# Kernel optimization log

Measured on AMD Instinct MI355X. Metric: run time of the kernel, lower is better.

## Reference

```python
import jax, jax.numpy as jnp
import numpy as np

L = 2        # num_hidden_layers
B = 2        # batch
S = 1024     # seq_len
D = 2048     # hidden_size
H = 32       # num_attention_heads
HD = D // H  # head_dim = 64
I = 8192     # intermediate_size
EPS = 1e-5
INIT = 0.02


def setup_inputs() -> dict:
    key = jax.random.key(0)
    ks = jax.random.split(key, 12)
    r = lambda k, shape: jax.random.normal(k, shape, dtype=jnp.float32) * INIT
    return {
        "hidden_states": jax.random.normal(ks[0], (B, S, D), dtype=jnp.float32),
        "attention_mask": jnp.ones((B, S), dtype=jnp.int32),
        "ln1_g": jnp.ones((L, D), jnp.float32),
        "ln1_b": jnp.zeros((L, D), jnp.float32),
        "qkv_w": r(ks[1], (L, D, 3 * D)),
        "o_w": r(ks[2], (L, D, D)),
        "ln2_g": jnp.ones((L, D), jnp.float32),
        "ln2_b": jnp.zeros((L, D), jnp.float32),
        "gu_w": r(ks[3], (L, D, 2 * I)),
        "gu_b": jnp.zeros((L, 2 * I), jnp.float32),
        "down_w": r(ks[4], (L, I, D)),
        "down_b": jnp.zeros((L, D), jnp.float32),
    }


def _layer_norm(x, g, b):
    mu = jnp.mean(x, axis=-1, keepdims=True)
    var = jnp.mean(jnp.square(x - mu), axis=-1, keepdims=True)
    return (x - mu) * jax.lax.rsqrt(var + EPS) * g + b


def _forward(hidden_states, attention_mask, ln1_g, ln1_b, qkv_w, o_w,
             ln2_g, ln2_b, gu_w, gu_b, down_w, down_b):
    # mask bias: (1 - mask) * -1e4, broadcast to [B, 1, 1, S]
    mask_bias = (1.0 - attention_mask.astype(jnp.float32))[:, None, None, :] * -10000.0
    scale = 1.0 / np.sqrt(HD)

    def layer(h, p):
        l1g, l1b, qw, ow, l2g, l2b, guw, gub, dw, db = p
        # --- attention block ---
        x = _layer_norm(h, l1g, l1b)
        qkv = jnp.einsum("bsd,de->bse", x, qw)                 # [B,S,3D]
        qkv = qkv.reshape(B, S, 3, H, HD).transpose(2, 0, 3, 1, 4)  # [3,B,H,S,HD]
        q, k, v = qkv[0], qkv[1], qkv[2]
        scores = jnp.einsum("bhqd,bhkd->bhqk", q, k) * scale + mask_bias
        attn = jax.nn.softmax(scores, axis=-1)
        ctx = jnp.einsum("bhqk,bhkd->bhqd", attn, v)           # [B,H,S,HD]
        ctx = ctx.transpose(0, 2, 1, 3).reshape(B, S, D)
        h = h + jnp.einsum("bsd,de->bse", ctx, ow)
        # --- MLP block (SwiGLU) ---
        y = _layer_norm(h, l2g, l2b)
        gu = jnp.einsum("bsd,de->bse", y, guw) + gub           # [B,S,2I]
        gate, up = gu[..., :I], gu[..., I:]
        mlp = jnp.einsum("bsi,id->bsd", jax.nn.swish(gate) * up, dw) + db
        return h + mlp, None

    params = (ln1_g, ln1_b, qkv_w, o_w, ln2_g, ln2_b, gu_w, gu_b, down_w, down_b)
    out, _ = jax.lax.scan(layer, hidden_states, params)
    return out


def reference(hidden_states, attention_mask, ln1_g, ln1_b, qkv_w, o_w,
              ln2_g, ln2_b, gu_w, gu_b, down_w, down_b):
    return _forward(hidden_states, attention_mask, ln1_g, ln1_b, qkv_w, o_w,
                    ln2_g, ln2_b, gu_w, gu_b, down_w, down_b)
```

## Files before the change

### kernel.cpp

```cpp
#include <hip/hip_runtime.h>

#define LNUM 2
#define BBATCH 2
#define SSEQ 1024
#define DDIM 2048
#define HHEADS 32
#define HDIM 64
#define IDIM 8192
#define MM 2048

typedef __attribute__((ext_vector_type(4))) float f32x4;
typedef __attribute__((ext_vector_type(8))) __bf16 bf16x8;
typedef __attribute__((ext_vector_type(4))) unsigned short us4;
typedef __attribute__((ext_vector_type(8))) unsigned short us8;

__device__ __forceinline__ unsigned short f2bf(float f) {
  union { float f; unsigned u; } v; v.f = f;
  unsigned r = v.u + 0x7fffu + ((v.u >> 16) & 1u);
  return (unsigned short)(r >> 16);
}
__device__ __forceinline__ float bf2f(unsigned short b) {
  union { unsigned u; float f; } v; v.u = ((unsigned)b) << 16;
  return v.f;
}

#define GLD16(g, l) __builtin_amdgcn_global_load_lds( \
    (const __attribute__((address_space(1))) void*)(g), \
    (__attribute__((address_space(3))) void*)(l), 16, 0, 0)

template<int REDSPLIT>
__global__ __launch_bounds__(256) void ln_kernel(
    float* __restrict__ x, const float* __restrict__ part,
    const float* __restrict__ rbias,
    const float* __restrict__ g, const float* __restrict__ bta,
    unsigned short* __restrict__ out)
{
  int tid = threadIdx.x;
  int lane = tid & 63, w = tid >> 6;
  int row = blockIdx.x;
  float* xr = x + (size_t)row * DDIM;
  f32x4* xr4 = (f32x4*)xr;
  f32x4 v[2];
  float s1 = 0.f, s2 = 0.f;
#pragma unroll
  for (int i = 0; i < 2; i++) {
    int idx4 = tid + 256 * i;
    v[i] = xr4[idx4];
    if (REDSPLIT > 0) {
#pragma unroll
      for (int s = 0; s < REDSPLIT; s++) {
        f32x4 p = *(const f32x4*)(part + (size_t)s * MM * DDIM + (size_t)row * DDIM + idx4 * 4);
        v[i] += p;
      }
      if (rbias) {
        f32x4 bv = *(const f32x4*)(rbias + idx4 * 4);
        v[i] += bv;
      }
      xr4[idx4] = v[i];
    }
#pragma unroll
    for (int j = 0; j < 4; j++) { s1 += v[i][j]; s2 += v[i][j] * v[i][j]; }
  }
#pragma unroll
  for (int m = 1; m < 64; m <<= 1) {
    s1 += __shfl_xor(s1, m);
    s2 += __shfl_xor(s2, m);
  }
  __shared__ float red[8];
  if (lane == 0) { red[w * 2] = s1; red[w * 2 + 1] = s2; }
  __syncthreads();
  s1 = red[0] + red[2] + red[4] + red[6];
  s2 = red[1] + red[3] + red[5] + red[7];
  float mu = s1 / (float)DDIM;
  float var = s2 / (float)DDIM - mu * mu;
  float rstd = rsqrtf(var + 1e-5f);
#pragma unroll
  for (int i = 0; i < 2; i++) {
    int c0 = (tid + 256 * i) * 4;
    us4 o;
#pragma unroll
    for (int j = 0; j < 4; j++)
      o[j] = f2bf((v[i][j] - mu) * rstd * g[c0 + j] + bta[c0 + j]);
    *(us4*)(out + (size_t)row * DDIM + c0) = o;
  }
}

__global__ __launch_bounds__(256) void red_kernel(
    float* __restrict__ out, const float* __restrict__ part,
    const float* __restrict__ bias)
{
  size_t i = (size_t)blockIdx.x * 256 + threadIdx.x;
  f32x4 o = ((f32x4*)out)[i];
#pragma unroll
  for (int s = 0; s < 4; s++)
    o += *(const f32x4*)(part + (size_t)s * MM * DDIM + i * 4);
  int col4 = (int)((i * 4) & (DDIM - 1));
  f32x4 bv = *(const f32x4*)(bias + col4);
  o += bv;
  ((f32x4*)out)[i] = o;
}

template<int PERM>
__global__ __launch_bounds__(256) void cvt_t_kernel(
    const float* __restrict__ W, unsigned short* __restrict__ Wt, int K, int N)
{
  __shared__ float tile[32][33];
  int t = threadIdx.x;
  int k0 = blockIdx.x << 5, n0 = blockIdx.y << 5;
  int r = t >> 3, c4 = (t & 7) << 2;
  int colbase;
  if (PERM == 1)
    colbase = (n0 >> 1) + (c4 & 15) + ((c4 & 16) ? (N >> 1) : 0);
  else
    colbase = n0 + c4;
  f32x4 v = *(const f32x4*)(W + (size_t)(k0 + r) * N + colbase);
  tile[r][c4 + 0] = v[0]; tile[r][c4 + 1] = v[1];
  tile[r][c4 + 2] = v[2]; tile[r][c4 + 3] = v[3];
  __syncthreads();
  us4 o;
#pragma unroll
  for (int j = 0; j < 4; j++) o[j] = f2bf(tile[c4 + j][r]);
  *(us4*)(Wt + (size_t)(n0 + r) * K + k0 + c4) = o;
}

template<int OUTMODE>
__global__ __launch_bounds__(256) void gemm_kernel(
    const unsigned short* __restrict__ A, const unsigned short* __restrict__ Bt,
    unsigned short* __restrict__ outB, float* __restrict__ outF,
    const float* __restrict__ bias, int M, int N, int K)
{
  __shared__ unsigned short As[128 * 32];
  __shared__ unsigned short Bs[128 * 32];
  int tid = threadIdx.x;
  int lane = tid & 63, w = tid >> 6;
  int m0 = blockIdx.y * 128, n0 = blockIdx.x * 128;
  int wr = w >> 1, wc = w & 1;

  f32x4 z4 = {0.f, 0.f, 0.f, 0.f};
  f32x4 acc[4][4];
#pragma unroll
  for (int i = 0; i < 4; i++)
#pragma unroll
    for (int j = 0; j < 4; j++) acc[i][j] = z4;

  int bofs0 = w * 1024 + lane * 16;
  int bofs1 = (4 + w) * 1024 + lane * 16;
  int r0 = bofs0 >> 6, c0 = (bofs0 & 63) >> 1;
  int r1 = bofs1 >> 6, c1 = (bofs1 & 63) >> 1;
  const unsigned short* a0 = A + (size_t)(m0 + r0) * K + c0;
  const unsigned short* a1 = A + (size_t)(m0 + r1) * K + c1;
  const unsigned short* b0 = Bt + (size_t)(n0 + r0) * K + c0;
  const unsigned short* b1 = Bt + (size_t)(n0 + r1) * K + c1;
  unsigned short* lA0 = As + w * 512;
  unsigned short* lA1 = As + (4 + w) * 512;
  unsigned short* lB0 = Bs + w * 512;
  unsigned short* lB1 = Bs + (4 + w) * 512;

  int arow = wr * 64 + (lane & 15);
  int brow = wc * 64 + (lane & 15);
  int koff = (lane >> 4) * 8;

  for (int kt = 0; kt < K; kt += 32) {
    __syncthreads();
    GLD16(a0 + kt, lA0);
    GLD16(a1 + kt, lA1);
    GLD16(b0 + kt, lB0);
    GLD16(b1 + kt, lB1);
    __syncthreads();
    bf16x8 af[4], bfr[4];
#pragma unroll
    for (int i = 0; i < 4; i++)
      af[i] = *(const bf16x8*)(As + (arow + i * 16) * 32 + koff);
#pragma unroll
    for (int j = 0; j < 4; j++)
      bfr[j] = *(const bf16x8*)(Bs + (brow + j * 16) * 32 + koff);
#pragma unroll
    for (int i = 0; i < 4; i++)
#pragma unroll
      for (int j = 0; j < 4; j++)
        acc[i][j] = __builtin_amdgcn_mfma_f32_16x16x32_bf16(af[i], bfr[j], acc[i][j], 0, 0, 0);
  }

  int grp = lane >> 4, l = lane & 15;
#pragma unroll
  for (int mi = 0; mi < 4; mi++) {
#pragma unroll
    for (int nj = 0; nj < 4; nj++) {
      int col = n0 + wc * 64 + nj * 16 + l;
      float bv = bias ? bias[col] : 0.f;
#pragma unroll
      for (int r = 0; r < 4; r++) {
        int row = m0 + wr * 64 + mi * 16 + grp * 4 + r;
        float v = acc[mi][nj][r] + bv;
        if (OUTMODE == 2) outF[(size_t)row * N + col] += v;
        else outB[(size_t)row * N + col] = f2bf(v);
      }
    }
  }
}

#define BAR __builtin_amdgcn_s_barrier()
#define SCHED0 __builtin_amdgcn_sched_barrier(0)
#define LGKM0 { asm volatile("s_waitcnt lgkmcnt(0)" ::: "memory"); SCHED0; }
#define VMC4 { asm volatile("s_waitcnt vmcnt(4)" ::: "memory"); SCHED0; }
#define VMC0 { asm volatile("s_waitcnt vmcnt(0)" ::: "memory"); SCHED0; }

#define STG_A(p,h,t) { \
  GLD16(pA[h][0] + (size_t)(t)*64, smem + ldsA + (p)*32768 + (h)*16384); \
  GLD16(pA[h][1] + (size_t)(t)*64, smem + ldsA + (p)*32768 + (h)*16384 + 8192); }
#define STG_B(p,h,t) { \
  GLD16(pB[h][0] + (size_t)(t)*64, smem + ldsB + (p)*32768 + (h)*16384); \
  GLD16(pB[h][1] + (size_t)(t)*64, smem + ldsB + (p)*32768 + (h)*16384 + 8192); }

#define DSR_A(p, misel, ks) { \
  _Pragma("unroll") \
  for (int mi = 0; mi < 4; mi++) \
    af[mi] = *(const bf16x8*)(smem + (p)*32768 + aRd + ((misel)*64 + mi*16)*128 + ch[ks]); }
#define DSR_B(p, ks) { \
  _Pragma("unroll") \
  for (int nj = 0; nj < 4; nj++) \
    bfr[ks][nj] = *(const bf16x8*)(smem + (p)*32768 + bRd + nj*2048 + ch[ks]); }

#define MFMA16(misel, ks) { \
  _Pragma("unroll") \
  for (int mi = 0; mi < 4; mi++) \
    _Pragma("unroll") \
    for (int nj = 0; nj < 4; nj++) \
      acc[(misel)*4+mi][nj] = __builtin_amdgcn_mfma_f32_16x16x32_bf16( \
          af[mi], bfr[ks][nj], acc[(misel)*4+mi][nj], 0, 0, 0); }

#define TILE(p, t) { \
  DSR_A(p, 0, 0); DSR_B(p, 0); \
  if ((t)+1 < NT) STG_A(1-(p), 0, (t)+1); \
  SCHED0; BAR; LGKM0; \
  __builtin_amdgcn_s_setprio(1); MFMA16(0, 0); __builtin_amdgcn_s_setprio(0); \
  SCHED0; BAR; \
  DSR_A(p, 0, 1); DSR_B(p, 1); \
  if ((t)+1 < NT) STG_A(1-(p), 1, (t)+1); \
  SCHED0; BAR; LGKM0; \
  __builtin_amdgcn_s_setprio(1); MFMA16(0, 1); __builtin_amdgcn_s_setprio(0); \
  SCHED0; BAR; \
  DSR_A(p, 1, 0); \
  if ((t)+2 < NT) STG_B(p, 0, (t)+2); \
  SCHED0; BAR; LGKM0; \
  __builtin_amdgcn_s_setprio(1); MFMA16(1, 0); __builtin_amdgcn_s_setprio(0); \
  SCHED0; BAR; \
  DSR_A(p, 1, 1); \
  if ((t)+2 < NT) STG_B(p, 1, (t)+2); \
  SCHED0; BAR; LGKM0; \
  __builtin_amdgcn_s_setprio(1); MFMA16(1, 1); __builtin_amdgcn_s_setprio(0); \
  if ((t)+2 < NT) { VMC4; } else { VMC0; } \
  SCHED0; BAR; }

template<int OUTMODE>
__global__ __launch_bounds__(512, 2) void gemm256_kernel(
    const unsigned short* __restrict__ A, const unsigned short* __restrict__ Bt,
    unsigned short* __restrict__ outB, float* __restrict__ outF,
    const float* __restrict__ bias, int M, int N, int Kstride, int Kc)
{
  extern __shared__ char smem[];
  int tid = threadIdx.x;
  int lane = tid & 63, w = tid >> 6;
  int wr = w >> 2, wc = w & 3;
  int l15 = lane & 15, grp = lane >> 4;

  int nwg = gridDim.x * gridDim.y;
  int bid = blockIdx.y * gridDim.x + blockIdx.x;
  int cpx = nwg >> 3;
  int sw = (bid & 7) * cpx + (bid >> 3);
  int bx = sw % gridDim.x, by = sw / gridDim.x;
  int m0 = by * 256, n0 = bx * 256;

  int NT = Kc >> 6;
  const unsigned short* Az = A  + (size_t)blockIdx.z * Kc;
  const unsigned short* Bz = Bt + (size_t)blockIdx.z * Kc;

  int srow = lane >> 3;
  int kcol = ((lane & 7) ^ srow) * 8;
  const unsigned short* pA[2][2];
  const unsigned short* pB[2][2];
#pragma unroll
  for (int h = 0; h < 2; h++)
#pragma unroll
    for (int i = 0; i < 2; i++) {
      pA[h][i] = Az + (size_t)(m0 + h*128 + i*64 + w*8 + srow) * Kstride + kcol;
      pB[h][i] = Bz + (size_t)(n0 + h*128 + i*64 + w*8 + srow) * Kstride + kcol;
    }
  int ldsA = w*1024 + lane*16;
  int ldsB = 65536 + w*1024 + lane*16;

  int aRd = (wr*128 + l15) * 128;
  int bRd = 65536 + (wc*64 + l15) * 128;
  int ch[2];
  ch[0] = ((0*4 + grp) ^ (l15 & 7)) * 16;
  ch[1] = ((1*4 + grp) ^ (l15 & 7)) * 16;

  f32x4 z4 = {0.f, 0.f, 0.f, 0.f};
  f32x4 acc[8][4];
#pragma unroll
  for (int i = 0; i < 8; i++)
#pragma unroll
    for (int j = 0; j < 4; j++) acc[i][j] = z4;
  bf16x8 af[4];
  bf16x8 bfr[2][4];

  STG_A(0, 0, 0); STG_A(0, 1, 0); STG_B(0, 0, 0); STG_B(0, 1, 0);
  if (NT > 1) { STG_B(1, 0, 1); STG_B(1, 1, 1); VMC4; } else { VMC0; }
  BAR;

  for (int t = 0; t < NT; t += 2) {
    TILE(0, t);
    TILE(1, t + 1);
  }

  if (OUTMODE == 3) {
    int cbase = n0 + wc * 64;
    int half = N >> 1;
#pragma unroll
    for (int mi = 0; mi < 8; mi++) {
#pragma unroll
      for (int p = 0; p < 2; p++) {
        int jcol = (cbase >> 1) + p * 16 + l15;
        float bg = bias[jcol];
        float bu = bias[half + jcol];
#pragma unroll
        for (int r = 0; r < 4; r++) {
          int row = m0 + wr * 128 + mi * 16 + grp * 4 + r;
          float g = acc[mi][2 * p][r] + bg;
          float u = acc[mi][2 * p + 1][r] + bu;
          float sv = g / (1.f + __expf(-g)) * u;
          outB[(size_t)row * half + jcol] = f2bf(sv);
        }
      }
    }
  } else {
#pragma unroll
    for (int mi = 0; mi < 8; mi++) {
#pragma unroll
      for (int nj = 0; nj < 4; nj++) {
        int col = n0 + wc * 64 + nj * 16 + l15;
        float bv = (OUTMODE == 0 && bias) ? bias[col] : 0.f;
#pragma unroll
        for (int r = 0; r < 4; r++) {
          int row = m0 + wr * 128 + mi * 16 + grp * 4 + r;
          float v = acc[mi][nj][r] + bv;
          if (OUTMODE == 1)
            outF[(size_t)blockIdx.z * M * N + (size_t)row * N + col] = v;
          else
            outB[(size_t)row * N + col] = f2bf(v);
        }
      }
    }
  }
}

__global__ __launch_bounds__(256) void attn_kernel(
    const unsigned short* __restrict__ qkv, const int* __restrict__ amask,
    unsigned short* __restrict__ ctx)
{
  __shared__ unsigned short Qs[128 * 80];
  __shared__ unsigned short Ks[128 * 80];
  __shared__ unsigned short Vt[64 * 144];
  __shared__ unsigned short Ps[128 * 80];

  int tid = threadIdx.x, lane = tid & 63, w = tid >> 6;
  int grp = lane >> 4, l = lane & 15;
  int q0 = blockIdx.x * 128;
  int bh = blockIdx.y;
  int b = bh >> 5, h = bh & 31;
  const size_t rs = 3 * DDIM;
  const unsigned short* qbase = qkv + (size_t)(b * SSEQ) * rs + h * HDIM;
  const unsigned short* kbase = qbase + DDIM;
  const unsigned short* vbase = qbase + 2 * DDIM;

#pragma unroll
  for (int i = 0; i < 4; i++) {
    int c = tid + 256 * i;
    int r = c >> 3, part = c & 7;
    us8 v = *(const us8*)(qbase + (size_t)(q0 + r) * rs + part * 8);
    *(us8*)(Qs + r * 80 + part * 8) = v;
  }

  float mrun[2][4], lrun[2][4];
  f32x4 z4 = {0.f, 0.f, 0.f, 0.f};
  f32x4 oacc[2][4];
#pragma unroll
  for (int mi = 0; mi < 2; mi++)
#pragma unroll
    for (int r = 0; r < 4; r++) { mrun[mi][r] = -1e30f; lrun[mi][r] = 0.f; }
#pragma unroll
  for (int mi = 0; mi < 2; mi++)
#pragma unroll
    for (int nj = 0; nj < 4; nj++) oacc[mi][nj] = z4;

  for (int kb = 0; kb < 8; kb++) {
#pragma unroll
    for (int i = 0; i < 4; i++) {
      int c = tid + 256 * i;
      int r = c >> 3, part = c & 7;
      us8 v = *(const us8*)(kbase + (size_t)(kb * 128 + r) * rs + part * 8);
      *(us8*)(Ks + r * 80 + part * 8) = v;
    }
#pragma unroll
    for (int i = 0; i < 2; i++) {
      int bb = tid + 256 * i;
      int hb = bb & 15, sb = bb >> 4;
      int hd0 = hb * 4, s0 = sb * 4;
      us4 rv[4];
#pragma unroll
      for (int j = 0; j < 4; j++)
        rv[j] = *(const us4*)(vbase + (size_t)(kb * 128 + s0 + j) * rs + hd0);
      int s8 = s0 >> 3, rem = s0 & 7;
#pragma unroll
      for (int j2 = 0; j2 < 4; j2++) {
        int hd = hd0 + j2;
        us4 ov;
        ov[0] = rv[0][j2]; ov[1] = rv[1][j2]; ov[2] = rv[2][j2]; ov[3] = rv[3][j2];
        *(us4*)(Vt + hd * 144 + ((s8 ^ (hd >> 2)) * 8) + rem) = ov;
      }
    }
    __syncthreads();

    f32x4 sc[2][8];
#pragma unroll
    for (int mi = 0; mi < 2; mi++)
#pragma unroll
      for (int nj = 0; nj < 8; nj++) sc[mi][nj] = z4;
    __builtin_amdgcn_s_setprio(1);
#pragma unroll
    for (int ks = 0; ks < 2; ks++) {
      bf16x8 aq[2];
#pragma unroll
      for (int mi = 0; mi < 2; mi++)
        aq[mi] = *(const bf16x8*)(Qs + (w * 32 + mi * 16 + l) * 80 + ks * 32 + grp * 8);
#pragma unroll
      for (int nj = 0; nj < 8; nj++) {
        bf16x8 bk = *(const bf16x8*)(Ks + (nj * 16 + l) * 80 + ks * 32 + grp * 8);
#pragma unroll
        for (int mi = 0; mi < 2; mi++)
          sc[mi][nj] = __builtin_amdgcn_mfma_f32_16x16x32_bf16(aq[mi], bk, sc[mi][nj], 0, 0, 0);
      }
    }
    __builtin_amdgcn_s_setprio(0);
    float mb[8];
#pragma unroll
    for (int nj = 0; nj < 8; nj++) {
      int col = kb * 128 + nj * 16 + l;
      mb[nj] = (1.0f - (float)amask[b * SSEQ + col]) * -10000.0f;
    }
#pragma unroll
    for (int mi = 0; mi < 2; mi++)
#pragma unroll
      for (int nj = 0; nj < 8; nj++)
#pragma unroll
        for (int r = 0; r < 4; r++)
          sc[mi][nj][r] = sc[mi][nj][r] * 0.125f + mb[nj];

    float pm[2][4];
#pragma unroll
    for (int mi = 0; mi < 2; mi++)
#pragma unroll
      for (int r = 0; r < 4; r++) {
        float m = sc[mi][0][r];
#pragma unroll
        for (int nj = 1; nj < 8; nj++) m = fmaxf(m, sc[mi][nj][r]);
#pragma unroll
        for (int s = 1; s <= 8; s <<= 1) m = fmaxf(m, __shfl_xor(m, s));
        pm[mi][r] = m;
      }
    float corr[2][4];
#pragma unroll
    for (int mi = 0; mi < 2; mi++)
#pragma unroll
      for (int r = 0; r < 4; r++) {
        float nm = fmaxf(mrun[mi][r], pm[mi][r]);
        corr[mi][r] = __expf(mrun[mi][r] - nm);
        mrun[mi][r] = nm;
      }
    float rsum[2][4];
#pragma unroll
    for (int mi = 0; mi < 2; mi++)
#pragma unroll
      for (int r = 0; r < 4; r++) rsum[mi][r] = 0.f;
#pragma unroll
    for (int mi = 0; mi < 2; mi++)
#pragma unroll
      for (int nj = 0; nj < 8; nj++)
#pragma unroll
        for (int r = 0; r < 4; r++) {
          float p = __expf(sc[mi][nj][r] - mrun[mi][r]);
          sc[mi][nj][r] = p;
          rsum[mi][r] += p;
        }
#pragma unroll
    for (int mi = 0; mi < 2; mi++)
#pragma unroll
      for (int r = 0; r < 4; r++) {
        float s = rsum[mi][r];
#pragma unroll
        for (int m = 1; m <= 8; m <<= 1) s += __shfl_xor(s, m);
        lrun[mi][r] = lrun[mi][r] * corr[mi][r] + s;
      }
#pragma unroll
    for (int mi = 0; mi < 2; mi++)
#pragma unroll
      for (int nj = 0; nj < 4; nj++)
#pragma unroll
        for (int r = 0; r < 4; r++) oacc[mi][nj][r] *= corr[mi][r];

#pragma unroll
    for (int h2 = 0; h2 < 2; h2++) {
#pragma unroll
      for (int mi = 0; mi < 2; mi++)
#pragma unroll
        for (int njl = 0; njl < 4; njl++)
#pragma unroll
          for (int r = 0; r < 4; r++)
            Ps[(w * 32 + mi * 16 + grp * 4 + r) * 80 + njl * 16 + l] =
                f2bf(sc[mi][h2 * 4 + njl][r]);
      __syncthreads();
      __builtin_amdgcn_s_setprio(1);
#pragma unroll
      for (int ksl = 0; ksl < 2; ksl++) {
        bf16x8 pf[2];
#pragma unroll
        for (int mi = 0; mi < 2; mi++)
          pf[mi] = *(const bf16x8*)(Ps + (w * 32 + mi * 16 + l) * 80 + ksl * 32 + grp * 8);
        int s8 = (h2 * 2 + ksl) * 4 + grp;
#pragma unroll
        for (int nj = 0; nj < 4; nj++) {
          int hd = nj * 16 + l;
          bf16x8 vf = *(const bf16x8*)(Vt + hd * 144 + ((s8 ^ (hd >> 2)) * 8));
#pragma unroll
          for (int mi = 0; mi < 2; mi++)
            oacc[mi][nj] = __builtin_amdgcn_mfma_f32_16x16x32_bf16(pf[mi], vf, oacc[mi][nj], 0, 0, 0);
        }
      }
      __builtin_amdgcn_s_setprio(0);
      __syncthreads();
    }
  }

#pragma unroll
  for (int mi = 0; mi < 2; mi++)
#pragma unroll
    for (int nj = 0; nj < 4; nj++)
#pragma unroll
      for (int r = 0; r < 4; r++) {
        int qrow = q0 + w * 32 + mi * 16 + grp * 4 + r;
        int hd = nj * 16 + l;
        float v = oacc[mi][nj][r] / lrun[mi][r];
        ctx[(size_t)(b * SSEQ + qrow) * DDIM + h * HDIM + hd] = f2bf(v);
      }
}

__global__ __launch_bounds__(256) void swiglu_kernel(
    const unsigned short* __restrict__ gu, unsigned short* __restrict__ a)
{
  size_t idx = ((size_t)blockIdx.x * 256 + threadIdx.x) * 8;
  int r = (int)(idx >> 13);
  int c = (int)(idx & 8191);
  const unsigned short* gp = gu + (size_t)r * (2 * IDIM) + c;
  us8 gv = *(const us8*)gp;
  us8 uv = *(const us8*)(gp + IDIM);
  us8 ov;
#pragma unroll
  for (int j = 0; j < 8; j++) {
    float g = bf2f(gv[j]), u = bf2f(uv[j]);
    ov[j] = f2bf(g / (1.f + __expf(-g)) * u);
  }
  *(us8*)(a + idx) = ov;
}

extern "C" void kernel_launch(void* const* d_in, const int* in_sizes, int n_in,
                              void* d_out, int out_size, void* d_ws, size_t ws_size,
                              hipStream_t stream) {
  (void)in_sizes; (void)n_in; (void)out_size; (void)ws_size;
  const float* hs    = (const float*)d_in[0];
  const int*   amask = (const int*)d_in[1];
  const float* ln1_g = (const float*)d_in[2];
  const float* ln1_b = (const float*)d_in[3];
  const float* qkv_w = (const float*)d_in[4];
  const float* o_w   = (const float*)d_in[5];
  const float* ln2_g = (const float*)d_in[6];
  const float* ln2_b = (const float*)d_in[7];
  const float* gu_w  = (const float*)d_in[8];
  const float* gu_b  = (const float*)d_in[9];
  const float* down_w = (const float*)d_in[10];
  const float* down_b = (const float*)d_in[11];
  float* out = (float*)d_out;

  char* ws = (char*)d_ws;
  unsigned short* Wt   = (unsigned short*)ws;
  unsigned short* xb   = (unsigned short*)(ws + 67108864);
  unsigned short* qkvb = (unsigned short*)(ws + 75497472);
  unsigned short* ctxb = (unsigned short*)(ws + 100663296);
  unsigned short* gub  = (unsigned short*)(ws + 109051904);
  unsigned short* ab   = qkvb;
  float* P = (float*)gub;

  hipError_t e0 = hipFuncSetAttribute(
      reinterpret_cast<const void*>(&gemm256_kernel<0>),
      hipFuncAttributeMaxDynamicSharedMemorySize, 131072);
  hipError_t e1 = hipFuncSetAttribute(
      reinterpret_cast<const void*>(&gemm256_kernel<1>),
      hipFuncAttributeMaxDynamicSharedMemorySize, 131072);
  hipError_t e3 = hipFuncSetAttribute(
      reinterpret_cast<const void*>(&gemm256_kernel<3>),
      hipFuncAttributeMaxDynamicSharedMemorySize, 131072);
  bool use256 = (e0 == hipSuccess && e1 == hipSuccess && e3 == hipSuccess);

  hipMemcpyAsync(out, hs, (size_t)MM * DDIM * sizeof(float),
                 hipMemcpyDeviceToDevice, stream);

  for (int lidx = 0; lidx < LNUM; lidx++) {
    if (use256 && lidx > 0)
      ln_kernel<4><<<MM, 256, 0, stream>>>(out, P, down_b + (lidx - 1) * DDIM,
          ln1_g + lidx * DDIM, ln1_b + lidx * DDIM, xb);
    else
      ln_kernel<0><<<MM, 256, 0, stream>>>(out, nullptr, nullptr,
          ln1_g + lidx * DDIM, ln1_b + lidx * DDIM, xb);

    cvt_t_kernel<0><<<dim3(DDIM / 32, (3 * DDIM) / 32), 256, 0, stream>>>(
        qkv_w + (size_t)lidx * DDIM * 3 * DDIM, Wt, DDIM, 3 * DDIM);
    if (use256)
      gemm256_kernel<0><<<dim3((3 * DDIM) / 256, MM / 256), 512, 131072, stream>>>(
          xb, Wt, qkvb, nullptr, nullptr, MM, 3 * DDIM, DDIM, DDIM);
    else
      gemm_kernel<0><<<dim3((3 * DDIM) / 128, MM / 128), 256, 0, stream>>>(
          xb, Wt, qkvb, nullptr, nullptr, MM, 3 * DDIM, DDIM);

    attn_kernel<<<dim3(SSEQ / 128, BBATCH * HHEADS), 256, 0, stream>>>(qkvb, amask, ctxb);

    cvt_t_kernel<0><<<dim3(DDIM / 32, DDIM / 32), 256, 0, stream>>>(
        o_w + (size_t)lidx * DDIM * DDIM, Wt, DDIM, DDIM);
    if (use256) {
      gemm256_kernel<1><<<dim3(DDIM / 256, MM / 256, 4), 512, 131072, stream>>>(
          ctxb, Wt, nullptr, P, nullptr, MM, DDIM, DDIM, DDIM / 4);
      ln_kernel<4><<<MM, 256, 0, stream>>>(out, P, nullptr,
          ln2_g + lidx * DDIM, ln2_b + lidx * DDIM, xb);
    } else {
      gemm_kernel<2><<<dim3(DDIM / 128, MM / 128), 256, 0, stream>>>(
          ctxb, Wt, nullptr, out, nullptr, MM, DDIM, DDIM);
      ln_kernel<0><<<MM, 256, 0, stream>>>(out, nullptr, nullptr,
          ln2_g + lidx * DDIM, ln2_b + lidx * DDIM, xb);
    }

    if (use256) {
      cvt_t_kernel<1><<<dim3(DDIM / 32, (2 * IDIM) / 32), 256, 0, stream>>>(
          gu_w + (size_t)lidx * DDIM * 2 * IDIM, Wt, DDIM, 2 * IDIM);
      gemm256_kernel<3><<<dim3((2 * IDIM) / 256, MM / 256), 512, 131072, stream>>>(
          xb, Wt, ab, nullptr, gu_b + (size_t)lidx * 2 * IDIM, MM, 2 * IDIM, DDIM, DDIM);
    } else {
      cvt_t_kernel<0><<<dim3(DDIM / 32, (2 * IDIM) / 32), 256, 0, stream>>>(
          gu_w + (size_t)lidx * DDIM * 2 * IDIM, Wt, DDIM, 2 * IDIM);
      gemm_kernel<0><<<dim3((2 * IDIM) / 128, MM / 128), 256, 0, stream>>>(
          xb, Wt, gub, nullptr, gu_b + (size_t)lidx * 2 * IDIM, MM, 2 * IDIM, DDIM);
      swiglu_kernel<<<(MM * IDIM / 8) / 256, 256, 0, stream>>>(gub, ab);
    }

    cvt_t_kernel<0><<<dim3(IDIM / 32, DDIM / 32), 256, 0, stream>>>(
        down_w + (size_t)lidx * IDIM * DDIM, Wt, IDIM, DDIM);
    if (use256) {
      gemm256_kernel<1><<<dim3(DDIM / 256, MM / 256, 4), 512, 131072, stream>>>(
          ab, Wt, nullptr, P, nullptr, MM, DDIM, IDIM, IDIM / 4);
      if (lidx == LNUM - 1)
        red_kernel<<<(MM * DDIM / 4) / 256, 256, 0, stream>>>(
            out, P, down_b + lidx * DDIM);
    } else {
      gemm_kernel<2><<<dim3(DDIM / 128, MM / 128), 256, 0, stream>>>(
          ab, Wt, nullptr, out, down_b + lidx * DDIM, MM, DDIM, IDIM);
    }
  }
}
```

Baseline: 952.2 us.

## Store split-K partials in bf16 and remap GEMM tiles per XCD by column

The split-K GEMM partial outputs are now written and read as bf16 rather than fp32, which halves the traffic for the partial buffers written by the GEMMs and summed in the layernorm and reduce kernels. The block-to-tile mapping is also changed so that each XCD owns a contiguous range of output columns and walks the rows, aiming for better L2 reuse of weight tiles. Rounding the partials to bf16 before summing adds precision error to the residual stream.

New measurement: 911.2 us. 4.3% less time.

```diff
diff --git a/kernel.cpp b/kernel.cpp
--- a/kernel.cpp
+++ b/kernel.cpp
@@ -30,7 +30,7 @@
 
 template<int REDSPLIT>
 __global__ __launch_bounds__(256) void ln_kernel(
-    float* __restrict__ x, const float* __restrict__ part,
+    float* __restrict__ x, const unsigned short* __restrict__ part,
     const float* __restrict__ rbias,
     const float* __restrict__ g, const float* __restrict__ bta,
     unsigned short* __restrict__ out)
@@ -49,8 +49,9 @@
     if (REDSPLIT > 0) {
 #pragma unroll
       for (int s = 0; s < REDSPLIT; s++) {
-        f32x4 p = *(const f32x4*)(part + (size_t)s * MM * DDIM + (size_t)row * DDIM + idx4 * 4);
-        v[i] += p;
+        us4 p = *(const us4*)(part + (size_t)s * MM * DDIM + (size_t)row * DDIM + idx4 * 4);
+#pragma unroll
+        for (int j = 0; j < 4; j++) v[i][j] += bf2f(p[j]);
       }
       if (rbias) {
         f32x4 bv = *(const f32x4*)(rbias + idx4 * 4);
@@ -86,14 +87,17 @@
 }
 
 __global__ __launch_bounds__(256) void red_kernel(
-    float* __restrict__ out, const float* __restrict__ part,
+    float* __restrict__ out, const unsigned short* __restrict__ part,
     const float* __restrict__ bias)
 {
   size_t i = (size_t)blockIdx.x * 256 + threadIdx.x;
   f32x4 o = ((f32x4*)out)[i];
 #pragma unroll
-  for (int s = 0; s < 4; s++)
-    o += *(const f32x4*)(part + (size_t)s * MM * DDIM + i * 4);
+  for (int s = 0; s < 4; s++) {
+    us4 p = *(const us4*)(part + (size_t)s * MM * DDIM + i * 4);
+#pragma unroll
+    for (int j = 0; j < 4; j++) o[j] += bf2f(p[j]);
+  }
   int col4 = (int)((i * 4) & (DDIM - 1));
   f32x4 bv = *(const f32x4*)(bias + col4);
   o += bv;
@@ -264,11 +268,12 @@
   int wr = w >> 2, wc = w & 3;
   int l15 = lane & 15, grp = lane >> 4;
 
-  int nwg = gridDim.x * gridDim.y;
-  int bid = blockIdx.y * gridDim.x + blockIdx.x;
-  int cpx = nwg >> 3;
-  int sw = (bid & 7) * cpx + (bid >> 3);
-  int bx = sw % gridDim.x, by = sw / gridDim.x;
+  int GX = gridDim.x, GY = gridDim.y;
+  int bid = blockIdx.y * GX + blockIdx.x;
+  int xcd = bid & 7;
+  int local = bid >> 3;
+  int bx = xcd * (GX >> 3) + local / GY;
+  int by = local % GY;
   int m0 = by * 256, n0 = bx * 256;
 
   int NT = Kc >> 6;
@@ -345,13 +350,14 @@
           int row = m0 + wr * 128 + mi * 16 + grp * 4 + r;
           float v = acc[mi][nj][r] + bv;
           if (OUTMODE == 1)
-            outF[(size_t)blockIdx.z * M * N + (size_t)row * N + col] = v;
+            outB[(size_t)blockIdx.z * M * N + (size_t)row * N + col] = f2bf(v);
           else
             outB[(size_t)row * N + col] = f2bf(v);
         }
       }
     }
   }
+  (void)outF;
 }
 
 __global__ __launch_bounds__(256) void attn_kernel(
@@ -597,7 +603,7 @@
   unsigned short* ctxb = (unsigned short*)(ws + 100663296);
   unsigned short* gub  = (unsigned short*)(ws + 109051904);
   unsigned short* ab   = qkvb;
-  float* P = (float*)gub;
+  unsigned short* P = gub;
 
   hipError_t e0 = hipFuncSetAttribute(
       reinterpret_cast<const void*>(&gemm256_kernel<0>),
@@ -636,7 +642,7 @@
         o_w + (size_t)lidx * DDIM * DDIM, Wt, DDIM, DDIM);
     if (use256) {
       gemm256_kernel<1><<<dim3(DDIM / 256, MM / 256, 4), 512, 131072, stream>>>(
-          ctxb, Wt, nullptr, P, nullptr, MM, DDIM, DDIM, DDIM / 4);
+          ctxb, Wt, P, nullptr, nullptr, MM, DDIM, DDIM, DDIM / 4);
       ln_kernel<4><<<MM, 256, 0, stream>>>(out, P, nullptr,
           ln2_g + lidx * DDIM, ln2_b + lidx * DDIM, xb);
     } else {
@@ -663,7 +669,7 @@
         down_w + (size_t)lidx * IDIM * DDIM, Wt, IDIM, DDIM);
     if (use256) {
       gemm256_kernel<1><<<dim3(DDIM / 256, MM / 256, 4), 512, 131072, stream>>>(
-          ab, Wt, nullptr, P, nullptr, MM, DDIM, IDIM, IDIM / 4);
+          ab, Wt, P, nullptr, nullptr, MM, DDIM, IDIM, IDIM / 4);
       if (lidx == LNUM - 1)
         red_kernel<<<(MM * DDIM / 4) / 256, 256, 0, stream>>>(
             out, P, down_b + lidx * DDIM);
```
